# Kernel optimization log

Measured on AMD Instinct MI355X. Metric: run time of the kernel, lower is better.

The kernel has to match this reference:

```python
import jax, jax.numpy as jnp
import numpy as np

N_USER, N_ITEM, N_REL = 200000, 100000, 64
DIM = 64
S_UU = S_UI = S_IU = S_II = 8
BATCH = 65536
MAX_RATING = 5.0


def setup_inputs() -> dict:
    key = jax.random.key(0)
    ks = jax.random.split(key, 24)
    inp = {}
    # query batch
    inp['u'] = jax.random.randint(ks[0], (BATCH,), 0, N_USER)
    inp['v'] = jax.random.randint(ks[1], (BATCH,), 0, N_ITEM)
    # embedding tables (init std=0.8 as in the torch code)
    inp['usr_feat'] = 0.8 * jax.random.normal(ks[2], (N_USER, DIM), jnp.float32)
    inp['item_feat'] = 0.8 * jax.random.normal(ks[3], (N_ITEM, DIM), jnp.float32)
    inp['rel_feat'] = 0.8 * jax.random.normal(ks[4], (N_REL, DIM), jnp.float32)
    # precomputed sampled neighbor tables (built once in __init__ in the original)
    inp['neigh_uu'] = jax.random.randint(ks[5], (N_USER, S_UU), 0, N_USER)
    inp['neigh_uu_st'] = jax.random.uniform(ks[6], (N_USER, S_UU), jnp.float32)
    inp['neigh_ui'] = jax.random.randint(ks[7], (N_USER, S_UI), 0, N_ITEM)
    inp['neigh_ui_rat'] = MAX_RATING * jax.random.uniform(ks[8], (N_USER, S_UI), jnp.float32)
    inp['neigh_ui_vot'] = jax.random.uniform(ks[9], (N_USER, S_UI), jnp.float32)
    inp['neigh_ui_tim'] = jax.random.uniform(ks[10], (N_USER, S_UI), jnp.float32)
    inp['neigh_iu'] = jax.random.randint(ks[11], (N_ITEM, S_IU), 0, N_USER)
    inp['neigh_iu_rat'] = MAX_RATING * jax.random.uniform(ks[12], (N_ITEM, S_IU), jnp.float32)
    inp['neigh_iu_vot'] = jax.random.uniform(ks[13], (N_ITEM, S_IU), jnp.float32)
    inp['neigh_iu_tim'] = jax.random.uniform(ks[14], (N_ITEM, S_IU), jnp.float32)
    inp['neigh_ii'] = jax.random.randint(ks[15], (N_ITEM, S_II), 0, N_ITEM)
    inp['neigh_ir'] = jax.random.randint(ks[16], (N_ITEM, S_II), 0, N_REL)
    # aggregator transforms (one per side)
    sc = 1.0 / np.sqrt(DIM)
    inp['Wu'] = sc * jax.random.normal(ks[17], (DIM, DIM), jnp.float32)
    inp['bu'] = jnp.zeros((DIM,), jnp.float32)
    inp['Wv'] = sc * jax.random.normal(ks[18], (DIM, DIM), jnp.float32)
    inp['bv'] = jnp.zeros((DIM,), jnp.float32)
    return inp


def reference(u, v, usr_feat, item_feat, rel_feat,
              neigh_uu, neigh_uu_st, neigh_ui, neigh_ui_rat, neigh_ui_vot, neigh_ui_tim,
              neigh_iu, neigh_iu_rat, neigh_iu_vot, neigh_iu_tim, neigh_ii, neigh_ir,
              Wu, bu, Wv, bv):
    u_emb = usr_feat[u]                                   # [B, D]
    v_emb = item_feat[v]                                  # [B, D]

    # ---- user-side aggregation ----
    # social neighbors, weighted by softmax over social tie strength
    uu_nei = usr_feat[neigh_uu[u]]                        # [B, S, D]
    w_uu = jax.nn.softmax(neigh_uu_st[u], axis=-1)        # [B, S]
    agg_uu = jnp.einsum('bs,bsd->bd', w_uu, uu_nei)
    # interacted items, weighted by rating * vote * time recency
    ui_nei = item_feat[neigh_ui[u]]                       # [B, S, D]
    s_ui = neigh_ui_rat[u] * neigh_ui_vot[u] * neigh_ui_tim[u]
    w_ui = jax.nn.softmax(s_ui, axis=-1)
    agg_ui = jnp.einsum('bs,bsd->bd', w_ui, ui_nei)
    user_h = jax.nn.relu((u_emb + agg_uu + agg_ui) @ Wu + bu)

    # ---- item-side aggregation ----
    # users who interacted with the item, weighted like above
    iu_nei = usr_feat[neigh_iu[v]]                        # [B, S, D]
    s_iu = neigh_iu_rat[v] * neigh_iu_vot[v] * neigh_iu_tim[v]
    w_iu = jax.nn.softmax(s_iu, axis=-1)
    agg_iu = jnp.einsum('bs,bsd->bd', w_iu, iu_nei)
    # KG neighbors with user-relation attention (KGCN-style)
    ii_nei = item_feat[neigh_ii[v]]                       # [B, S, D]
    rel = rel_feat[neigh_ir[v]]                           # [B, S, D]
    att = jnp.einsum('bd,bsd->bs', u_emb, rel)            # user-relation score
    w_ii = jax.nn.softmax(att, axis=-1)
    agg_ii = jnp.einsum('bs,bsd->bd', w_ii, ii_nei)
    item_h = jax.nn.relu((v_emb + agg_iu + agg_ii) @ Wv + bv)

    # rating prediction
    score = jax.nn.sigmoid(jnp.sum(user_h * item_h, axis=-1)) * MAX_RATING
    return score
```

## Files before the change

### kernel.cpp

```cpp
#include <hip/hip_runtime.h>
#include <math.h>

constexpr int DIM = 64;
constexpr int S = 8;
constexpr int WPB = 8;
constexpr int BLOCK = WPB * 64;
constexpr int GRID = 1024;
constexpr int WSTR = 68;

__device__ __forceinline__ void octet_softmax(float sc, float* wout) {
    float m = sc;
    m = fmaxf(m, __shfl_xor(m, 1));
    m = fmaxf(m, __shfl_xor(m, 2));
    m = fmaxf(m, __shfl_xor(m, 4));
    float e = __expf(sc - m);
    float s = e;
    s += __shfl_xor(s, 1);
    s += __shfl_xor(s, 2);
    s += __shfl_xor(s, 4);
    float w = e / s;
    #pragma unroll
    for (int k = 0; k < 8; k++) wout[k] = __shfl(w, k);
}

__global__ __launch_bounds__(BLOCK)
void sestkgcn_kernel(
    const int*   __restrict__ u_idx,
    const int*   __restrict__ v_idx,
    const float* __restrict__ usr_feat,
    const float* __restrict__ item_feat,
    const float* __restrict__ rel_feat,
    const int*   __restrict__ neigh_uu,
    const float* __restrict__ neigh_uu_st,
    const int*   __restrict__ neigh_ui,
    const float* __restrict__ neigh_ui_rat,
    const float* __restrict__ neigh_ui_vot,
    const float* __restrict__ neigh_ui_tim,
    const int*   __restrict__ neigh_iu,
    const float* __restrict__ neigh_iu_rat,
    const float* __restrict__ neigh_iu_vot,
    const float* __restrict__ neigh_iu_tim,
    const int*   __restrict__ neigh_ii,
    const int*   __restrict__ neigh_ir,
    const float* __restrict__ Wu,
    const float* __restrict__ bu,
    const float* __restrict__ Wv,
    const float* __restrict__ bv,
    float*       __restrict__ out,
    int n)
{
    __shared__ float sWuT[DIM * WSTR];
    __shared__ float sWvT[DIM * WSTR];
    __shared__ float sbu[DIM];
    __shared__ float sbv[DIM];
    __shared__ float xs[WPB * DIM];

    const int tid = threadIdx.x;
    for (int i = tid; i < DIM * DIM; i += BLOCK) {
        const int d_ = i >> 6, j_ = i & 63;
        sWuT[j_ * WSTR + d_] = Wu[i];
        sWvT[j_ * WSTR + d_] = Wv[i];
    }
    if (tid < DIM) { sbu[tid] = bu[tid]; sbv[tid] = bv[tid]; }
    __syncthreads();

    const int wave = tid >> 6;
    const int lane = tid & 63;
    const int ls   = lane & 7;

    float* xw = &xs[wave * DIM];
    const float4* wuT = (const float4*)&sWuT[lane * WSTR];
    const float4* wvT = (const float4*)&sWvT[lane * WSTR];
    const float4* xw4 = (const float4*)xw;
    const float bu_l = sbu[lane];
    const float bv_l = sbv[lane];

    const int stride = GRID * WPB;
    for (int b = blockIdx.x * WPB + wave; b < n; b += stride) {
        const int u = u_idx[b];
        const int v = v_idx[b];
        const unsigned u8 = (unsigned)u << 3, v8 = (unsigned)v << 3;
        const unsigned u64o = (unsigned)u << 6, v64o = (unsigned)v << 6;

        const float u_d = usr_feat[u64o | (unsigned)lane];
        const float v_d = item_feat[v64o | (unsigned)lane];

        const float sc_uu = neigh_uu_st[u8 + ls];
        const float sc_ui = neigh_ui_rat[u8 + ls] * neigh_ui_vot[u8 + ls] * neigh_ui_tim[u8 + ls];
        const float sc_iu = neigh_iu_rat[v8 + ls] * neigh_iu_vot[v8 + ls] * neigh_iu_tim[v8 + ls];

        float w[S];
        octet_softmax(sc_uu, w);
        float agg_uu = 0.f;
        {
            const int4 i0 = ((const int4*)(neigh_uu + u8))[0];
            const int4 i1 = ((const int4*)(neigh_uu + u8))[1];
            const int ni[S] = {i0.x, i0.y, i0.z, i0.w, i1.x, i1.y, i1.z, i1.w};
            float r[S];
            #pragma unroll
            for (int s = 0; s < S; s++) r[s] = usr_feat[((unsigned)ni[s] << 6) | (unsigned)lane];
            #pragma unroll
            for (int s = 0; s < S; s++) agg_uu = fmaf(w[s], r[s], agg_uu);
        }

        octet_softmax(sc_ui, w);
        float agg_ui = 0.f;
        {
            const int4 i0 = ((const int4*)(neigh_ui + u8))[0];
            const int4 i1 = ((const int4*)(neigh_ui + u8))[1];
            const int ni[S] = {i0.x, i0.y, i0.z, i0.w, i1.x, i1.y, i1.z, i1.w};
            float r[S];
            #pragma unroll
            for (int s = 0; s < S; s++) r[s] = item_feat[((unsigned)ni[s] << 6) | (unsigned)lane];
            #pragma unroll
            for (int s = 0; s < S; s++) agg_ui = fmaf(w[s], r[s], agg_ui);
        }

        float hu;
        {
            xw[lane] = u_d + agg_uu + agg_ui;
            __threadfence_block();
            float a0 = 0.f, a1 = 0.f, a2 = 0.f, a3 = 0.f;
            #pragma unroll
            for (int k = 0; k < DIM / 4; k++) {
                float4 xv = xw4[k];
                float4 wv = wuT[k];
                a0 = fmaf(xv.x, wv.x, a0);
                a1 = fmaf(xv.y, wv.y, a1);
                a2 = fmaf(xv.z, wv.z, a2);
                a3 = fmaf(xv.w, wv.w, a3);
            }
            hu = fmaxf((a0 + a1) + (a2 + a3) + bu_l, 0.f);
        }

        octet_softmax(sc_iu, w);
        float agg_iu = 0.f;
        {
            const int4 i0 = ((const int4*)(neigh_iu + v8))[0];
            const int4 i1 = ((const int4*)(neigh_iu + v8))[1];
            const int ni[S] = {i0.x, i0.y, i0.z, i0.w, i1.x, i1.y, i1.z, i1.w};
            float r[S];
            #pragma unroll
            for (int s = 0; s < S; s++) r[s] = usr_feat[((unsigned)ni[s] << 6) | (unsigned)lane];
            #pragma unroll
            for (int s = 0; s < S; s++) agg_iu = fmaf(w[s], r[s], agg_iu);
        }

        {
            const int4 r0 = ((const int4*)(neigh_ir + v8))[0];
            const int4 r1 = ((const int4*)(neigh_ir + v8))[1];
            const int nr[S] = {r0.x, r0.y, r0.z, r0.w, r1.x, r1.y, r1.z, r1.w};
            float p[S];
            #pragma unroll
            for (int s = 0; s < S; s++) p[s] = u_d * rel_feat[((unsigned)nr[s] << 6) | (unsigned)lane];

            float m1[4];
            #pragma unroll
            for (int i = 0; i < 4; i++) {
                float lo = (lane & 1) ? p[2 * i + 1] : p[2 * i];
                float hi = (lane & 1) ? p[2 * i]     : p[2 * i + 1];
                m1[i] = lo + __shfl_xor(hi, 1);
            }
            float m2[2];
            #pragma unroll
            for (int i = 0; i < 2; i++) {
                float lo = (lane & 2) ? m1[2 * i + 1] : m1[2 * i];
                float hi = (lane & 2) ? m1[2 * i]     : m1[2 * i + 1];
                m2[i] = lo + __shfl_xor(hi, 2);
            }
            float lo = (lane & 4) ? m2[1] : m2[0];
            float hi = (lane & 4) ? m2[0] : m2[1];
            float att = lo + __shfl_xor(hi, 4);
            att += __shfl_xor(att, 8);
            att += __shfl_xor(att, 16);
            att += __shfl_xor(att, 32);
            octet_softmax(att, w);
        }
        float agg_ii = 0.f;
        {
            const int4 i0 = ((const int4*)(neigh_ii + v8))[0];
            const int4 i1 = ((const int4*)(neigh_ii + v8))[1];
            const int ni[S] = {i0.x, i0.y, i0.z, i0.w, i1.x, i1.y, i1.z, i1.w};
            float r[S];
            #pragma unroll
            for (int s = 0; s < S; s++) r[s] = item_feat[((unsigned)ni[s] << 6) | (unsigned)lane];
            #pragma unroll
            for (int s = 0; s < S; s++) agg_ii = fmaf(w[s], r[s], agg_ii);
        }

        float hv;
        {
            xw[lane] = v_d + agg_iu + agg_ii;
            __threadfence_block();
            float a0 = 0.f, a1 = 0.f, a2 = 0.f, a3 = 0.f;
            #pragma unroll
            for (int k = 0; k < DIM / 4; k++) {
                float4 xv = xw4[k];
                float4 wv = wvT[k];
                a0 = fmaf(xv.x, wv.x, a0);
                a1 = fmaf(xv.y, wv.y, a1);
                a2 = fmaf(xv.z, wv.z, a2);
                a3 = fmaf(xv.w, wv.w, a3);
            }
            hv = fmaxf((a0 + a1) + (a2 + a3) + bv_l, 0.f);
        }

        float p = hu * hv;
        #pragma unroll
        for (int off = 32; off > 0; off >>= 1) p += __shfl_xor(p, off);
        if (lane == 0) out[b] = 5.0f / (1.0f + __expf(-p));
    }
}

extern "C" void kernel_launch(void* const* d_in, const int* in_sizes, int n_in,
                              void* d_out, int out_size, void* d_ws, size_t ws_size,
                              hipStream_t stream) {
    const int*   u_idx        = (const int*)  d_in[0];
    const int*   v_idx        = (const int*)  d_in[1];
    const float* usr_feat     = (const float*)d_in[2];
    const float* item_feat    = (const float*)d_in[3];
    const float* rel_feat     = (const float*)d_in[4];
    const int*   neigh_uu     = (const int*)  d_in[5];
    const float* neigh_uu_st  = (const float*)d_in[6];
    const int*   neigh_ui     = (const int*)  d_in[7];
    const float* neigh_ui_rat = (const float*)d_in[8];
    const float* neigh_ui_vot = (const float*)d_in[9];
    const float* neigh_ui_tim = (const float*)d_in[10];
    const int*   neigh_iu     = (const int*)  d_in[11];
    const float* neigh_iu_rat = (const float*)d_in[12];
    const float* neigh_iu_vot = (const float*)d_in[13];
    const float* neigh_iu_tim = (const float*)d_in[14];
    const int*   neigh_ii     = (const int*)  d_in[15];
    const int*   neigh_ir     = (const int*)  d_in[16];
    const float* Wu           = (const float*)d_in[17];
    const float* bu           = (const float*)d_in[18];
    const float* Wv           = (const float*)d_in[19];
    const float* bv           = (const float*)d_in[20];
    float*       out          = (float*)d_out;

    const int n = in_sizes[0];
    int blocks = (n + WPB - 1) / WPB;
    if (blocks > GRID) blocks = GRID;
    sestkgcn_kernel<<<blocks, BLOCK, 0, stream>>>(
        u_idx, v_idx, usr_feat, item_feat, rel_feat,
        neigh_uu, neigh_uu_st, neigh_ui, neigh_ui_rat, neigh_ui_vot, neigh_ui_tim,
        neigh_iu, neigh_iu_rat, neigh_iu_vot, neigh_iu_tim, neigh_ii, neigh_ir,
        Wu, bu, Wv, bv, out, n);
}
```

Measured before the change: 254.6 us.

## Prefetch next query indices, hoist neighbor index loads, use DPP swizzles

The grid-stride loop now loads the next iteration's u/v indices one step ahead, and all neighbor index int4 loads are issued up front so more gathers can be in flight at once. Lane xor-1 and xor-2 shuffles are replaced with DPP quad-permute moves, which avoid LDS-based ds_bpermute. Block size doubles to 16 waves with grid halved and an occupancy hint is added to launch bounds. Hoisting the loads raises register pressure, which may reduce occupancy or cause spills.

```diff
diff --git a/kernel.cpp b/kernel.cpp
--- a/kernel.cpp
+++ b/kernel.cpp
@@ -3,27 +3,35 @@
 
 constexpr int DIM = 64;
 constexpr int S = 8;
-constexpr int WPB = 8;
+constexpr int WPB = 16;
 constexpr int BLOCK = WPB * 64;
-constexpr int GRID = 1024;
+constexpr int GRID = 512;
 constexpr int WSTR = 68;
+
+template <int CTRL>
+__device__ __forceinline__ float dppx(float x) {
+    return __builtin_bit_cast(float,
+        __builtin_amdgcn_mov_dpp(__builtin_bit_cast(int, x), CTRL, 0xf, 0xf, true));
+}
+#define XOR1 0xB1
+#define XOR2 0x4E
 
 __device__ __forceinline__ void octet_softmax(float sc, float* wout) {
     float m = sc;
-    m = fmaxf(m, __shfl_xor(m, 1));
-    m = fmaxf(m, __shfl_xor(m, 2));
+    m = fmaxf(m, dppx<XOR1>(m));
+    m = fmaxf(m, dppx<XOR2>(m));
     m = fmaxf(m, __shfl_xor(m, 4));
     float e = __expf(sc - m);
     float s = e;
-    s += __shfl_xor(s, 1);
-    s += __shfl_xor(s, 2);
+    s += dppx<XOR1>(s);
+    s += dppx<XOR2>(s);
     s += __shfl_xor(s, 4);
     float w = e / s;
     #pragma unroll
     for (int k = 0; k < 8; k++) wout[k] = __shfl(w, k);
 }
 
-__global__ __launch_bounds__(BLOCK)
+__global__ __launch_bounds__(BLOCK, 8)
 void sestkgcn_kernel(
     const int*   __restrict__ u_idx,
     const int*   __restrict__ v_idx,
@@ -76,26 +84,46 @@
     const float bv_l = sbv[lane];
 
     const int stride = GRID * WPB;
-    for (int b = blockIdx.x * WPB + wave; b < n; b += stride) {
-        const int u = u_idx[b];
-        const int v = v_idx[b];
+    int b = blockIdx.x * WPB + wave;
+    if (b >= n) return;
+
+    int u = u_idx[b];
+    int v = v_idx[b];
+
+    while (b < n) {
+        const int b2 = b + stride;
+        const int bc = (b2 < n) ? b2 : b;
+        const int u_nxt = u_idx[bc];
+        const int v_nxt = v_idx[bc];
+
         const unsigned u8 = (unsigned)u << 3, v8 = (unsigned)v << 3;
-        const unsigned u64o = (unsigned)u << 6, v64o = (unsigned)v << 6;
-
-        const float u_d = usr_feat[u64o | (unsigned)lane];
-        const float v_d = item_feat[v64o | (unsigned)lane];
-
-        const float sc_uu = neigh_uu_st[u8 + ls];
-        const float sc_ui = neigh_ui_rat[u8 + ls] * neigh_ui_vot[u8 + ls] * neigh_ui_tim[u8 + ls];
-        const float sc_iu = neigh_iu_rat[v8 + ls] * neigh_iu_vot[v8 + ls] * neigh_iu_tim[v8 + ls];
+
+        const float u_d = usr_feat[((unsigned)u << 6) | (unsigned)lane];
+        const float v_d = item_feat[((unsigned)v << 6) | (unsigned)lane];
+
+        const float sc_uu_raw = neigh_uu_st[u8 + ls];
+        const float r_ui = neigh_ui_rat[u8 + ls], vo_ui = neigh_ui_vot[u8 + ls], t_ui = neigh_ui_tim[u8 + ls];
+        const float r_iu = neigh_iu_rat[v8 + ls], vo_iu = neigh_iu_vot[v8 + ls], t_iu = neigh_iu_tim[v8 + ls];
+
+        const int4 uu0 = ((const int4*)(neigh_uu + u8))[0];
+        const int4 uu1 = ((const int4*)(neigh_uu + u8))[1];
+        const int4 ui0 = ((const int4*)(neigh_ui + u8))[0];
+        const int4 ui1 = ((const int4*)(neigh_ui + u8))[1];
+        const int4 iu0 = ((const int4*)(neigh_iu + v8))[0];
+        const int4 iu1 = ((const int4*)(neigh_iu + v8))[1];
+        const int4 ii0 = ((const int4*)(neigh_ii + v8))[0];
+        const int4 ii1 = ((const int4*)(neigh_ii + v8))[1];
+        const int4 ir0 = ((const int4*)(neigh_ir + v8))[0];
+        const int4 ir1 = ((const int4*)(neigh_ir + v8))[1];
+
+        const float sc_ui = r_ui * vo_ui * t_ui;
+        const float sc_iu = r_iu * vo_iu * t_iu;
 
         float w[S];
-        octet_softmax(sc_uu, w);
+        octet_softmax(sc_uu_raw, w);
         float agg_uu = 0.f;
         {
-            const int4 i0 = ((const int4*)(neigh_uu + u8))[0];
-            const int4 i1 = ((const int4*)(neigh_uu + u8))[1];
-            const int ni[S] = {i0.x, i0.y, i0.z, i0.w, i1.x, i1.y, i1.z, i1.w};
+            const int ni[S] = {uu0.x, uu0.y, uu0.z, uu0.w, uu1.x, uu1.y, uu1.z, uu1.w};
             float r[S];
             #pragma unroll
             for (int s = 0; s < S; s++) r[s] = usr_feat[((unsigned)ni[s] << 6) | (unsigned)lane];
@@ -106,9 +134,7 @@
         octet_softmax(sc_ui, w);
         float agg_ui = 0.f;
         {
-            const int4 i0 = ((const int4*)(neigh_ui + u8))[0];
-            const int4 i1 = ((const int4*)(neigh_ui + u8))[1];
-            const int ni[S] = {i0.x, i0.y, i0.z, i0.w, i1.x, i1.y, i1.z, i1.w};
+            const int ni[S] = {ui0.x, ui0.y, ui0.z, ui0.w, ui1.x, ui1.y, ui1.z, ui1.w};
             float r[S];
             #pragma unroll
             for (int s = 0; s < S; s++) r[s] = item_feat[((unsigned)ni[s] << 6) | (unsigned)lane];
@@ -136,9 +162,7 @@
         octet_softmax(sc_iu, w);
         float agg_iu = 0.f;
         {
-            const int4 i0 = ((const int4*)(neigh_iu + v8))[0];
-            const int4 i1 = ((const int4*)(neigh_iu + v8))[1];
-            const int ni[S] = {i0.x, i0.y, i0.z, i0.w, i1.x, i1.y, i1.z, i1.w};
+            const int ni[S] = {iu0.x, iu0.y, iu0.z, iu0.w, iu1.x, iu1.y, iu1.z, iu1.w};
             float r[S];
             #pragma unroll
             for (int s = 0; s < S; s++) r[s] = usr_feat[((unsigned)ni[s] << 6) | (unsigned)lane];
@@ -147,9 +171,7 @@
         }
 
         {
-            const int4 r0 = ((const int4*)(neigh_ir + v8))[0];
-            const int4 r1 = ((const int4*)(neigh_ir + v8))[1];
-            const int nr[S] = {r0.x, r0.y, r0.z, r0.w, r1.x, r1.y, r1.z, r1.w};
+            const int nr[S] = {ir0.x, ir0.y, ir0.z, ir0.w, ir1.x, ir1.y, ir1.z, ir1.w};
             float p[S];
             #pragma unroll
             for (int s = 0; s < S; s++) p[s] = u_d * rel_feat[((unsigned)nr[s] << 6) | (unsigned)lane];
@@ -159,14 +181,14 @@
             for (int i = 0; i < 4; i++) {
                 float lo = (lane & 1) ? p[2 * i + 1] : p[2 * i];
                 float hi = (lane & 1) ? p[2 * i]     : p[2 * i + 1];
-                m1[i] = lo + __shfl_xor(hi, 1);
+                m1[i] = lo + dppx<XOR1>(hi);
             }
             float m2[2];
             #pragma unroll
             for (int i = 0; i < 2; i++) {
                 float lo = (lane & 2) ? m1[2 * i + 1] : m1[2 * i];
                 float hi = (lane & 2) ? m1[2 * i]     : m1[2 * i + 1];
-                m2[i] = lo + __shfl_xor(hi, 2);
+                m2[i] = lo + dppx<XOR2>(hi);
             }
             float lo = (lane & 4) ? m2[1] : m2[0];
             float hi = (lane & 4) ? m2[0] : m2[1];
@@ -178,9 +200,7 @@
         }
         float agg_ii = 0.f;
         {
-            const int4 i0 = ((const int4*)(neigh_ii + v8))[0];
-            const int4 i1 = ((const int4*)(neigh_ii + v8))[1];
-            const int ni[S] = {i0.x, i0.y, i0.z, i0.w, i1.x, i1.y, i1.z, i1.w};
+            const int ni[S] = {ii0.x, ii0.y, ii0.z, ii0.w, ii1.x, ii1.y, ii1.z, ii1.w};
             float r[S];
             #pragma unroll
             for (int s = 0; s < S; s++) r[s] = item_feat[((unsigned)ni[s] << 6) | (unsigned)lane];
@@ -190,6 +210,7 @@
 
         float hv;
         {
+            __threadfence_block();
             xw[lane] = v_d + agg_iu + agg_ii;
             __threadfence_block();
             float a0 = 0.f, a1 = 0.f, a2 = 0.f, a3 = 0.f;
@@ -206,9 +227,17 @@
         }
 
         float p = hu * hv;
-        #pragma unroll
-        for (int off = 32; off > 0; off >>= 1) p += __shfl_xor(p, off);
+        p += dppx<XOR1>(p);
+        p += dppx<XOR2>(p);
+        p += __shfl_xor(p, 4);
+        p += __shfl_xor(p, 8);
+        p += __shfl_xor(p, 16);
+        p += __shfl_xor(p, 32);
         if (lane == 0) out[b] = 5.0f / (1.0f + __expf(-p));
+
+        b = b2;
+        u = u_nxt;
+        v = v_nxt;
     }
 }
 
```

Result: slower. 316.8 us (+24.4%).
